# Kernel tuning notes

Measured on AMD Instinct MI355X. Metric: run time of the kernel, lower is better.

## Reference

```python
import jax, jax.numpy as jnp
import numpy as np

N, E, F, H, C, G = 100000, 1000000, 64, 64, 10, 256


def setup_inputs() -> dict:
    key = jax.random.key(0)
    ks = jax.random.split(key, 16)
    s = 1.0 / np.sqrt(F)
    sh = 1.0 / np.sqrt(H)
    return {
        "x": jax.random.normal(ks[0], (N, F), dtype=jnp.float32),
        "edge_index": jax.random.randint(ks[1], (2, E), 0, N, dtype=jnp.int32),
        "edge_attr": jax.random.uniform(ks[2], (E,), dtype=jnp.float32),
        "batch": jnp.sort(jax.random.randint(ks[3], (N,), 0, G, dtype=jnp.int32)),
        "W1r": jax.random.uniform(ks[4], (F, H), minval=-s, maxval=s),
        "W1s": jax.random.uniform(ks[5], (F, H), minval=-s, maxval=s),
        "b1": jax.random.uniform(ks[6], (H,), minval=-s, maxval=s),
        "W2r": jax.random.uniform(ks[7], (H, H), minval=-sh, maxval=sh),
        "W2s": jax.random.uniform(ks[8], (H, H), minval=-sh, maxval=sh),
        "b2": jax.random.uniform(ks[9], (H,), minval=-sh, maxval=sh),
        "W3r": jax.random.uniform(ks[10], (H, H), minval=-sh, maxval=sh),
        "W3s": jax.random.uniform(ks[11], (H, H), minval=-sh, maxval=sh),
        "b3": jax.random.uniform(ks[12], (H,), minval=-sh, maxval=sh),
        "Wl": jax.random.uniform(ks[13], (H, C), minval=-sh, maxval=sh),
        "bl": jax.random.uniform(ks[14], (C,), minval=-sh, maxval=sh),
    }


def graph_conv(x, src, dst, ew, W_rel, W_root, b):
    # gather neighbor feats, weight per-edge, scatter-add to destination
    msgs = x[src] * ew[:, None]                              # [E, F]
    agg = jax.ops.segment_sum(msgs, dst, num_segments=N)     # [N, F]
    return agg @ W_rel + x @ W_root + b                      # [N, H]


def reference(x, edge_index, edge_attr, batch,
              W1r, W1s, b1, W2r, W2s, b2, W3r, W3s, b3, Wl, bl):
    src, dst = edge_index[0], edge_index[1]
    h = jax.nn.relu(graph_conv(x, src, dst, edge_attr, W1r, W1s, b1))
    h = jax.nn.relu(graph_conv(h, src, dst, edge_attr, W2r, W2s, b2))
    h = jax.nn.relu(graph_conv(h, src, dst, edge_attr, W3r, W3s, b3))
    # global mean pool over graphs in the batch
    sums = jax.ops.segment_sum(h, batch, num_segments=G)      # [G, H]
    cnts = jax.ops.segment_sum(jnp.ones((N,), h.dtype), batch, num_segments=G)
    pooled = sums / jnp.maximum(cnts, 1.0)[:, None]
    # dropout is identity in eval mode
    return pooled @ Wl + bl                                   # [G, C]
```

## Files before the change

kernel.cpp:

```cpp
#include <hip/hip_runtime.h>


#define GCN_F 64
#define GCN_C 10
#define CB_SHIFT 9
#define CB_NODES 512
#define NCB_MAX 200
#define CAP 7168
#define SC_CHUNK 2048

typedef __attribute__((ext_vector_type(8))) short bf16x8;
typedef __attribute__((ext_vector_type(4))) float f32x4;

__device__ __forceinline__ unsigned short f2b(float v) {
    union { float f; unsigned int u; } c; c.f = v;
    unsigned int u = c.u;
    return (unsigned short)((u + 0x7FFFu + ((u >> 16) & 1u)) >> 16);
}
__device__ __forceinline__ float b2f(unsigned short u) {
    union { unsigned int u; float f; } c; c.u = ((unsigned int)u) << 16; return c.f;
}

__global__ __launch_bounds__(256) void cvtz_kernel(const float* __restrict__ in,
                                                   unsigned short* __restrict__ out,
                                                   int n4, int* __restrict__ zp, int zn) {
    int gid = blockIdx.x * 256 + threadIdx.x;
    if (gid < zn) zp[gid] = 0;
    int stride = gridDim.x * 256;
    for (int i = gid; i < n4; i += stride) {
        float4 v = reinterpret_cast<const float4*>(in)[i];
        ushort4 o;
        o.x = f2b(v.x); o.y = f2b(v.y); o.z = f2b(v.z); o.w = f2b(v.w);
        reinterpret_cast<ushort4*>(out)[i] = o;
    }
}

__global__ __launch_bounds__(256) void histC_kernel(const int* __restrict__ dst,
                                                    int* __restrict__ bcnt,
                                                    int E, int NCB) {
    __shared__ int h[NCB_MAX];
    int tid = threadIdx.x;
    for (int i = tid; i < NCB; i += 256) h[i] = 0;
    __syncthreads();
    int e0 = blockIdx.x * 4096 + tid;
#pragma unroll
    for (int k = 0; k < 16; ++k) {
        int e = e0 + k * 256;
        if (e < E) atomicAdd(&h[dst[e] >> CB_SHIFT], 1);
    }
    __syncthreads();
    for (int i = tid; i < NCB; i += 256)
        if (h[i]) atomicAdd(&bcnt[i], h[i]);
}

__global__ void bscan_kernel(const int* __restrict__ bcnt, int* __restrict__ gstart,
                             int nb) {
    int lane = threadIdx.x;
    int carry = 0;
    for (int base = 0; base < nb; base += 64) {
        int i = base + lane;
        int v = (i < nb) ? bcnt[i] : 0;
        int sc = v;
#pragma unroll
        for (int off = 1; off < 64; off <<= 1) {
            int t = __shfl_up(sc, off);
            if (lane >= off) sc += t;
        }
        if (i < nb) gstart[i] = carry + sc - v;
        carry += __shfl(sc, 63);
    }
    if (lane == 0) gstart[nb] = carry;
}

__global__ __launch_bounds__(256) void scatterC_kernel(
    const int* __restrict__ src, const int* __restrict__ dst,
    const float* __restrict__ ew, const int* __restrict__ gstart,
    int* __restrict__ gcursor, int2* __restrict__ ebufA, int E, int NCB) {
    __shared__ int2 recS[SC_CHUNK];
    __shared__ int gdest[SC_CHUNK];
    __shared__ int hist[NCB_MAX];
    __shared__ int lstart[NCB_MAX];
    __shared__ int gbase[NCB_MAX];
    __shared__ int cur[NCB_MAX];
    __shared__ int sb[256];

    int tid = threadIdx.x;
    int base = blockIdx.x * SC_CHUNK;
    int m = min(SC_CHUNK, E - base);

    for (int i = tid; i < NCB; i += 256) hist[i] = 0;
    __syncthreads();

    int2 rec[8];
    int bk[8];
#pragma unroll
    for (int k = 0; k < 8; ++k) {
        int e = base + k * 256 + tid;
        if (e < E) {
            int d = dst[e];
            bk[k] = d >> CB_SHIFT;
            rec[k] = make_int2(src[e] | ((d & (CB_NODES - 1)) << 17),
                               __float_as_int(ew[e]));
            atomicAdd(&hist[bk[k]], 1);
        } else bk[k] = -1;
    }
    __syncthreads();

    int v = (tid < NCB) ? hist[tid] : 0;
    sb[tid] = v;
    __syncthreads();
    for (int o = 1; o < 256; o <<= 1) {
        int t = (tid >= o) ? sb[tid - o] : 0;
        __syncthreads();
        sb[tid] += t;
        __syncthreads();
    }
    if (tid < NCB) {
        int excl = sb[tid] - v;
        lstart[tid] = excl;
        cur[tid] = excl;
        gbase[tid] = (v > 0) ? atomicAdd(&gcursor[tid], v) : 0;
    }
    __syncthreads();

#pragma unroll
    for (int k = 0; k < 8; ++k) {
        if (bk[k] >= 0) {
            int p = atomicAdd(&cur[bk[k]], 1);
            recS[p] = rec[k];
            gdest[p] = gstart[bk[k]] + gbase[bk[k]] + (p - lstart[bk[k]]);
        }
    }
    __syncthreads();

    for (int i = tid; i < m; i += 256) ebufA[gdest[i]] = recS[i];
}

__global__ __launch_bounds__(256) void sortCB_kernel(
    const int2* __restrict__ ebufA, const int* __restrict__ gstart,
    int2* __restrict__ ebufS, int* __restrict__ offsets, int N, int E) {
    __shared__ int2 rec[CAP];
    __shared__ int cnt[CB_NODES];
    __shared__ int cur[CB_NODES];
    __shared__ int sbuf[256];
    int cb = blockIdx.x, tid = threadIdx.x;
    int e0 = gstart[cb], e1 = gstart[cb + 1];
    int m = min(e1 - e0, CAP);

    for (int i = tid; i < m; i += 256) rec[i] = ebufA[e0 + i];
    for (int i = tid; i < CB_NODES; i += 256) cnt[i] = 0;
    __syncthreads();
    for (int i = tid; i < m; i += 256)
        atomicAdd(&cnt[(unsigned)rec[i].x >> 17], 1);
    __syncthreads();

    int c0 = cnt[2 * tid], c1 = cnt[2 * tid + 1];
    int part = c0 + c1;
    sbuf[tid] = part;
    __syncthreads();
    for (int off = 1; off < 256; off <<= 1) {
        int t = (tid >= off) ? sbuf[tid - off] : 0;
        __syncthreads();
        sbuf[tid] += t;
        __syncthreads();
    }
    int excl = sbuf[tid] - part;
    int pre0 = excl, pre1 = excl + c0;
    cur[2 * tid] = pre0;
    cur[2 * tid + 1] = pre1;
    int g0 = cb * CB_NODES + 2 * tid;
    if (g0 <= N)     offsets[g0]     = e0 + pre0;
    if (g0 + 1 <= N) offsets[g0 + 1] = e0 + pre1;
    __syncthreads();

    for (int i = tid; i < m; i += 256) {
        int d9 = (unsigned)rec[i].x >> 17;
        int pos = atomicAdd(&cur[d9], 1);
        ebufS[e0 + pos] = make_int2(rec[i].x & 0x1FFFF, rec[i].y);
    }
}

__global__ __launch_bounds__(512) void layer_kernel(
    const unsigned short* __restrict__ xin, const int* __restrict__ offsets,
    const int2* __restrict__ ebufS, const float* __restrict__ Wr,
    const float* __restrict__ Ws, const float* __restrict__ b,
    unsigned short* __restrict__ out, int n)
{
    __shared__ __align__(16) unsigned short bfrag[2][2][4][64][8];
    __shared__ __align__(16) unsigned short aggS[8][16][72];
    int tid = threadIdx.x, lane = tid & 63, wave = tid >> 6;

    for (int i = tid; i < 8192; i += 512) {
        int op = i >> 12;
        int ks = (i >> 11) & 1;
        int ct = (i >> 9) & 3;
        int l  = (i >> 3) & 63;
        int j  = i & 7;
        int k   = ks * 32 + (l >> 4) * 8 + j;
        int col = ct * 16 + (l & 15);
        const float* W = op ? Ws : Wr;
        ((unsigned short*)bfrag)[i] = f2b(W[k * GCN_F + col]);
    }
    __syncthreads();

    int l8 = lane & 7;
    int grp = lane >> 3;
    int gbase = (lane & 56) << 2;
    int wbase = blockIdx.x * 128 + wave * 16;

#pragma unroll
    for (int half = 0; half < 2; ++half) {
        int node = wbase + half * 8 + grp;
        bool nv = node < n;
        int p0 = 0, p1 = 0;
        if (nv) { p0 = offsets[node]; p1 = offsets[node + 1]; }
        float acc[8] = {0.f, 0.f, 0.f, 0.f, 0.f, 0.f, 0.f, 0.f};

        int idx = p0 + l8;
        bool v = idx < p1;
        if (__any(v)) {
            int2 er = ebufS[v ? idx : 0];
            int s  = v ? er.x : 0;
            int wb = v ? er.y : 0;

            for (int c = 1;; ++c) {
                int idxn = p0 + c * 8 + l8;
                bool vn = idxn < p1;
                int2 ern = ebufS[vn ? idxn : 0];

                int sj[8], wj[8];
#pragma unroll
                for (int j = 0; j < 8; ++j) {
                    sj[j] = __builtin_amdgcn_ds_bpermute(gbase + (j << 2), s);
                    wj[j] = __builtin_amdgcn_ds_bpermute(gbase + (j << 2), wb);
                }
                int4 r[8];
#pragma unroll
                for (int j = 0; j < 8; ++j)
                    r[j] = *reinterpret_cast<const int4*>(
                        xin + ((size_t)sj[j] << 6) + l8 * 8);
#pragma unroll
                for (int j = 0; j < 8; ++j) {
                    float wf = __int_as_float(wj[j]);
                    acc[0] = fmaf(__int_as_float(r[j].x << 16),        wf, acc[0]);
                    acc[1] = fmaf(__int_as_float(r[j].x & 0xFFFF0000), wf, acc[1]);
                    acc[2] = fmaf(__int_as_float(r[j].y << 16),        wf, acc[2]);
                    acc[3] = fmaf(__int_as_float(r[j].y & 0xFFFF0000), wf, acc[3]);
                    acc[4] = fmaf(__int_as_float(r[j].z << 16),        wf, acc[4]);
                    acc[5] = fmaf(__int_as_float(r[j].z & 0xFFFF0000), wf, acc[5]);
                    acc[6] = fmaf(__int_as_float(r[j].w << 16),        wf, acc[6]);
                    acc[7] = fmaf(__int_as_float(r[j].w & 0xFFFF0000), wf, acc[7]);
                }

                if (!__any(vn)) break;
                s  = vn ? ern.x : 0;
                wb = vn ? ern.y : 0;
            }
        }

        int4 o;
        o.x = (int)f2b(acc[0]) | ((int)f2b(acc[1]) << 16);
        o.y = (int)f2b(acc[2]) | ((int)f2b(acc[3]) << 16);
        o.z = (int)f2b(acc[4]) | ((int)f2b(acc[5]) << 16);
        o.w = (int)f2b(acc[6]) | ((int)f2b(acc[7]) << 16);
        *reinterpret_cast<int4*>(&aggS[wave][half * 8 + grp][l8 * 8]) = o;
    }

    int l15 = lane & 15, lhi = lane >> 4;

    bf16x8 B[2][2][4];
#pragma unroll
    for (int op = 0; op < 2; ++op)
#pragma unroll
        for (int ks = 0; ks < 2; ++ks)
#pragma unroll
            for (int ct = 0; ct < 4; ++ct)
                B[op][ks][ct] = *reinterpret_cast<const bf16x8*>(&bfrag[op][ks][ct][lane][0]);

    float bias[4];
#pragma unroll
    for (int ct = 0; ct < 4; ++ct) bias[ct] = b[ct * 16 + l15];

    bf16x8 a0 = *reinterpret_cast<const bf16x8*>(&aggS[wave][l15][lhi * 8]);
    bf16x8 a1 = *reinterpret_cast<const bf16x8*>(&aggS[wave][l15][32 + lhi * 8]);
    const unsigned short* xp = xin + (size_t)min(wbase + l15, n - 1) * GCN_F + lhi * 8;
    bf16x8 x0 = *reinterpret_cast<const bf16x8*>(xp);
    bf16x8 x1 = *reinterpret_cast<const bf16x8*>(xp + 32);

#pragma unroll
    for (int ct = 0; ct < 4; ++ct) {
        f32x4 acc = {0.f, 0.f, 0.f, 0.f};
        acc = __builtin_amdgcn_mfma_f32_16x16x32_bf16(a0, B[0][0][ct], acc, 0, 0, 0);
        acc = __builtin_amdgcn_mfma_f32_16x16x32_bf16(a1, B[0][1][ct], acc, 0, 0, 0);
        acc = __builtin_amdgcn_mfma_f32_16x16x32_bf16(x0, B[1][0][ct], acc, 0, 0, 0);
        acc = __builtin_amdgcn_mfma_f32_16x16x32_bf16(x1, B[1][1][ct], acc, 0, 0, 0);
        int col = ct * 16 + l15;
#pragma unroll
        for (int r = 0; r < 4; ++r) {
            int orow = wbase + lhi * 4 + r;
            if (orow < n) {
                float v = fmaxf(acc[r] + bias[ct], 0.f);
                out[(size_t)orow * GCN_F + col] = f2b(v);
            }
        }
    }
}

__global__ __launch_bounds__(256) void pool_kernel(
    const unsigned short* __restrict__ h, const int* __restrict__ batch,
    const float* __restrict__ Wl, const float* __restrict__ bl,
    float* __restrict__ out, int n)
{
    int g    = blockIdx.x;
    int tid  = threadIdx.x;
    int lane = tid & 63;
    int wave = tid >> 6;

    int i0, i1;
    {
        int lo = 0, hi = n;
        while (lo < hi) { int mid = (lo + hi) >> 1; if (batch[mid] < g) lo = mid + 1; else hi = mid; }
        i0 = lo;
        lo = i0; hi = n;
        while (lo < hi) { int mid = (lo + hi) >> 1; if (batch[mid] < g + 1) lo = mid + 1; else hi = mid; }
        i1 = lo;
    }

    float s = 0.f;
    for (int i = i0 + wave; i < i1; i += 4) s += b2f(h[(size_t)i * GCN_F + lane]);

    __shared__ float sp[4][GCN_F];
    sp[wave][lane] = s;
    __syncthreads();
    if (wave == 0) {
        float tot = sp[0][lane] + sp[1][lane] + sp[2][lane] + sp[3][lane];
        float cntf = (float)(i1 - i0);
        sp[0][lane] = tot / fmaxf(cntf, 1.f);
    }
    __syncthreads();
    if (tid < GCN_C) {
        float o = bl[tid];
#pragma unroll
        for (int j = 0; j < GCN_F; ++j) o += sp[0][j] * Wl[j * GCN_C + tid];
        out[g * GCN_C + tid] = o;
    }
}

extern "C" void kernel_launch(void* const* d_in, const int* in_sizes, int n_in,
                              void* d_out, int out_size, void* d_ws, size_t ws_size,
                              hipStream_t stream) {
    const float* x     = (const float*)d_in[0];
    const int*   ei    = (const int*)d_in[1];
    const float* ew    = (const float*)d_in[2];
    const int*   batch = (const int*)d_in[3];
    const float* W1r   = (const float*)d_in[4];
    const float* W1s   = (const float*)d_in[5];
    const float* b1    = (const float*)d_in[6];
    const float* W2r   = (const float*)d_in[7];
    const float* W2s   = (const float*)d_in[8];
    const float* b2    = (const float*)d_in[9];
    const float* W3r   = (const float*)d_in[10];
    const float* W3s   = (const float*)d_in[11];
    const float* b3    = (const float*)d_in[12];
    const float* Wl    = (const float*)d_in[13];
    const float* bl    = (const float*)d_in[14];
    float* out = (float*)d_out;

    const int N = in_sizes[0] / GCN_F;
    const int E = in_sizes[2];
    const int G = out_size / GCN_C;
    const int NCB = (N + CB_NODES - 1) / CB_NODES;

    const int* src = ei;
    const int* dst = ei + E;

    char* ws = (char*)d_ws;
    size_t off = 0;
    size_t csz = ((size_t)NCB * 4 + 15) & ~(size_t)15;
    int* bcnt    = (int*)(ws + off);  off += csz;
    int* gcursor = (int*)(ws + off);  off += csz;
    int* gstart  = (int*)(ws + off);  off += ((size_t)(NCB + 1) * 4 + 15) & ~(size_t)15;
    int* offsets = (int*)(ws + off);  off += ((size_t)(N + 1) * 4 + 15) & ~(size_t)15;
    int2* ebufA  = (int2*)(ws + off); off += (size_t)E * 8;
    int2* ebufS  = (int2*)(ws + off); off += (size_t)E * 8;
    unsigned short* buf0 = (unsigned short*)(ws + off); off += (size_t)N * GCN_F * 2;
    unsigned short* buf1 = (unsigned short*)(ws + off); off += (size_t)N * GCN_F * 2;

    int hblocks = (E + 4095) / 4096;
    int sblocks = (E + SC_CHUNK - 1) / SC_CHUNK;
    int zcount  = (int)(csz * 2 / 4);

    cvtz_kernel<<<1024, 256, 0, stream>>>(x, buf0, N * GCN_F / 4, bcnt, zcount);
    histC_kernel<<<hblocks, 256, 0, stream>>>(dst, bcnt, E, NCB);
    bscan_kernel<<<1, 64, 0, stream>>>(bcnt, gstart, NCB);
    scatterC_kernel<<<sblocks, 256, 0, stream>>>(src, dst, ew, gstart, gcursor, ebufA, E, NCB);
    sortCB_kernel<<<NCB, 256, 0, stream>>>(ebufA, gstart, ebufS, offsets, N, E);

    const int LBLK = (N + 127) / 128;
    layer_kernel<<<LBLK, 512, 0, stream>>>(buf0, offsets, ebufS, W1r, W1s, b1, buf1, N);
    layer_kernel<<<LBLK, 512, 0, stream>>>(buf1, offsets, ebufS, W2r, W2s, b2, buf0, N);
    layer_kernel<<<LBLK, 512, 0, stream>>>(buf0, offsets, ebufS, W3r, W3s, b3, buf1, N);

    pool_kernel<<<G, 256, 0, stream>>>(buf1, batch, Wl, bl, out, N);
}
```

Before: 233.1 us.

## Drop histogram/scan with fixed-capacity buckets and persistent work-stealing layer kernel

Removes the histogram and scan kernels by giving each 512-node destination bucket a fixed CAP-sized slot, so the scatter kernel uses only per-bucket atomic cursors and sortCB records each bucket's end. The layer kernel becomes persistent: 768 blocks whose waves pull 16-node groups from a global atomic counter, which balances uneven degrees and cuts block launch overhead. The intent is fewer launches in preprocessing and better load balance during aggregation. The cost is extra atomics and a padded edge buffer, and a bucket holding more than CAP edges would silently drop edges (the old code also capped at CAP).

```diff
diff --git a/kernel.cpp b/kernel.cpp
--- a/kernel.cpp
+++ b/kernel.cpp
@@ -35,46 +35,9 @@
     }
 }
 
-__global__ __launch_bounds__(256) void histC_kernel(const int* __restrict__ dst,
-                                                    int* __restrict__ bcnt,
-                                                    int E, int NCB) {
-    __shared__ int h[NCB_MAX];
-    int tid = threadIdx.x;
-    for (int i = tid; i < NCB; i += 256) h[i] = 0;
-    __syncthreads();
-    int e0 = blockIdx.x * 4096 + tid;
-#pragma unroll
-    for (int k = 0; k < 16; ++k) {
-        int e = e0 + k * 256;
-        if (e < E) atomicAdd(&h[dst[e] >> CB_SHIFT], 1);
-    }
-    __syncthreads();
-    for (int i = tid; i < NCB; i += 256)
-        if (h[i]) atomicAdd(&bcnt[i], h[i]);
-}
-
-__global__ void bscan_kernel(const int* __restrict__ bcnt, int* __restrict__ gstart,
-                             int nb) {
-    int lane = threadIdx.x;
-    int carry = 0;
-    for (int base = 0; base < nb; base += 64) {
-        int i = base + lane;
-        int v = (i < nb) ? bcnt[i] : 0;
-        int sc = v;
-#pragma unroll
-        for (int off = 1; off < 64; off <<= 1) {
-            int t = __shfl_up(sc, off);
-            if (lane >= off) sc += t;
-        }
-        if (i < nb) gstart[i] = carry + sc - v;
-        carry += __shfl(sc, 63);
-    }
-    if (lane == 0) gstart[nb] = carry;
-}
-
 __global__ __launch_bounds__(256) void scatterC_kernel(
     const int* __restrict__ src, const int* __restrict__ dst,
-    const float* __restrict__ ew, const int* __restrict__ gstart,
+    const float* __restrict__ ew,
     int* __restrict__ gcursor, int2* __restrict__ ebufA, int E, int NCB) {
     __shared__ int2 recS[SC_CHUNK];
     __shared__ int gdest[SC_CHUNK];
@@ -128,7 +91,7 @@
         if (bk[k] >= 0) {
             int p = atomicAdd(&cur[bk[k]], 1);
             recS[p] = rec[k];
-            gdest[p] = gstart[bk[k]] + gbase[bk[k]] + (p - lstart[bk[k]]);
+            gdest[p] = bk[k] * CAP + gbase[bk[k]] + (p - lstart[bk[k]]);
         }
     }
     __syncthreads();
@@ -137,15 +100,17 @@
 }
 
 __global__ __launch_bounds__(256) void sortCB_kernel(
-    const int2* __restrict__ ebufA, const int* __restrict__ gstart,
-    int2* __restrict__ ebufS, int* __restrict__ offsets, int N, int E) {
+    const int2* __restrict__ ebufA, const int* __restrict__ gcursor,
+    int2* __restrict__ ebufS, int* __restrict__ offsets, int* __restrict__ bend,
+    int N, int E) {
     __shared__ int2 rec[CAP];
     __shared__ int cnt[CB_NODES];
     __shared__ int cur[CB_NODES];
     __shared__ int sbuf[256];
     int cb = blockIdx.x, tid = threadIdx.x;
-    int e0 = gstart[cb], e1 = gstart[cb + 1];
-    int m = min(e1 - e0, CAP);
+    int e0 = cb * CAP;
+    int m = min(gcursor[cb], CAP);
+    if (tid == 0) bend[cb] = e0 + m;
 
     for (int i = tid; i < m; i += 256) rec[i] = ebufA[e0 + i];
     for (int i = tid; i < CB_NODES; i += 256) cnt[i] = 0;
@@ -182,9 +147,10 @@
 
 __global__ __launch_bounds__(512) void layer_kernel(
     const unsigned short* __restrict__ xin, const int* __restrict__ offsets,
-    const int2* __restrict__ ebufS, const float* __restrict__ Wr,
-    const float* __restrict__ Ws, const float* __restrict__ b,
-    unsigned short* __restrict__ out, int n)
+    const int* __restrict__ bend, const int2* __restrict__ ebufS,
+    const float* __restrict__ Wr, const float* __restrict__ Ws,
+    const float* __restrict__ b, unsigned short* __restrict__ out,
+    int* __restrict__ stealc, int ngroups, int n)
 {
     __shared__ __align__(16) unsigned short bfrag[2][2][4][64][8];
     __shared__ __align__(16) unsigned short aggS[8][16][72];
@@ -206,66 +172,6 @@
     int l8 = lane & 7;
     int grp = lane >> 3;
     int gbase = (lane & 56) << 2;
-    int wbase = blockIdx.x * 128 + wave * 16;
-
-#pragma unroll
-    for (int half = 0; half < 2; ++half) {
-        int node = wbase + half * 8 + grp;
-        bool nv = node < n;
-        int p0 = 0, p1 = 0;
-        if (nv) { p0 = offsets[node]; p1 = offsets[node + 1]; }
-        float acc[8] = {0.f, 0.f, 0.f, 0.f, 0.f, 0.f, 0.f, 0.f};
-
-        int idx = p0 + l8;
-        bool v = idx < p1;
-        if (__any(v)) {
-            int2 er = ebufS[v ? idx : 0];
-            int s  = v ? er.x : 0;
-            int wb = v ? er.y : 0;
-
-            for (int c = 1;; ++c) {
-                int idxn = p0 + c * 8 + l8;
-                bool vn = idxn < p1;
-                int2 ern = ebufS[vn ? idxn : 0];
-
-                int sj[8], wj[8];
-#pragma unroll
-                for (int j = 0; j < 8; ++j) {
-                    sj[j] = __builtin_amdgcn_ds_bpermute(gbase + (j << 2), s);
-                    wj[j] = __builtin_amdgcn_ds_bpermute(gbase + (j << 2), wb);
-                }
-                int4 r[8];
-#pragma unroll
-                for (int j = 0; j < 8; ++j)
-                    r[j] = *reinterpret_cast<const int4*>(
-                        xin + ((size_t)sj[j] << 6) + l8 * 8);
-#pragma unroll
-                for (int j = 0; j < 8; ++j) {
-                    float wf = __int_as_float(wj[j]);
-                    acc[0] = fmaf(__int_as_float(r[j].x << 16),        wf, acc[0]);
-                    acc[1] = fmaf(__int_as_float(r[j].x & 0xFFFF0000), wf, acc[1]);
-                    acc[2] = fmaf(__int_as_float(r[j].y << 16),        wf, acc[2]);
-                    acc[3] = fmaf(__int_as_float(r[j].y & 0xFFFF0000), wf, acc[3]);
-                    acc[4] = fmaf(__int_as_float(r[j].z << 16),        wf, acc[4]);
-                    acc[5] = fmaf(__int_as_float(r[j].z & 0xFFFF0000), wf, acc[5]);
-                    acc[6] = fmaf(__int_as_float(r[j].w << 16),        wf, acc[6]);
-                    acc[7] = fmaf(__int_as_float(r[j].w & 0xFFFF0000), wf, acc[7]);
-                }
-
-                if (!__any(vn)) break;
-                s  = vn ? ern.x : 0;
-                wb = vn ? ern.y : 0;
-            }
-        }
-
-        int4 o;
-        o.x = (int)f2b(acc[0]) | ((int)f2b(acc[1]) << 16);
-        o.y = (int)f2b(acc[2]) | ((int)f2b(acc[3]) << 16);
-        o.z = (int)f2b(acc[4]) | ((int)f2b(acc[5]) << 16);
-        o.w = (int)f2b(acc[6]) | ((int)f2b(acc[7]) << 16);
-        *reinterpret_cast<int4*>(&aggS[wave][half * 8 + grp][l8 * 8]) = o;
-    }
-
     int l15 = lane & 15, lhi = lane >> 4;
 
     bf16x8 B[2][2][4];
@@ -281,26 +187,96 @@
 #pragma unroll
     for (int ct = 0; ct < 4; ++ct) bias[ct] = b[ct * 16 + l15];
 
-    bf16x8 a0 = *reinterpret_cast<const bf16x8*>(&aggS[wave][l15][lhi * 8]);
-    bf16x8 a1 = *reinterpret_cast<const bf16x8*>(&aggS[wave][l15][32 + lhi * 8]);
-    const unsigned short* xp = xin + (size_t)min(wbase + l15, n - 1) * GCN_F + lhi * 8;
-    bf16x8 x0 = *reinterpret_cast<const bf16x8*>(xp);
-    bf16x8 x1 = *reinterpret_cast<const bf16x8*>(xp + 32);
-
-#pragma unroll
-    for (int ct = 0; ct < 4; ++ct) {
-        f32x4 acc = {0.f, 0.f, 0.f, 0.f};
-        acc = __builtin_amdgcn_mfma_f32_16x16x32_bf16(a0, B[0][0][ct], acc, 0, 0, 0);
-        acc = __builtin_amdgcn_mfma_f32_16x16x32_bf16(a1, B[0][1][ct], acc, 0, 0, 0);
-        acc = __builtin_amdgcn_mfma_f32_16x16x32_bf16(x0, B[1][0][ct], acc, 0, 0, 0);
-        acc = __builtin_amdgcn_mfma_f32_16x16x32_bf16(x1, B[1][1][ct], acc, 0, 0, 0);
-        int col = ct * 16 + l15;
-#pragma unroll
-        for (int r = 0; r < 4; ++r) {
-            int orow = wbase + lhi * 4 + r;
-            if (orow < n) {
-                float v = fmaxf(acc[r] + bias[ct], 0.f);
-                out[(size_t)orow * GCN_F + col] = f2b(v);
+    for (;;) {
+        int gsel = 0;
+        if (lane == 0) gsel = atomicAdd(stealc, 1);
+        gsel = __builtin_amdgcn_readfirstlane(gsel);
+        if (gsel >= ngroups) break;
+        int wbase = gsel * 16;
+
+#pragma unroll
+        for (int half = 0; half < 2; ++half) {
+            int node = wbase + half * 8 + grp;
+            bool nv = node < n;
+            int p0 = 0, p1 = 0;
+            if (nv) {
+                p0 = offsets[node];
+                p1 = ((node & (CB_NODES - 1)) == CB_NODES - 1)
+                         ? bend[node >> CB_SHIFT] : offsets[node + 1];
+            }
+            float acc[8] = {0.f, 0.f, 0.f, 0.f, 0.f, 0.f, 0.f, 0.f};
+
+            int idx = p0 + l8;
+            bool v = idx < p1;
+            if (__any(v)) {
+                int2 er = ebufS[v ? idx : 0];
+                int s  = v ? er.x : 0;
+                int wb = v ? er.y : 0;
+
+                for (int c = 1;; ++c) {
+                    int idxn = p0 + c * 8 + l8;
+                    bool vn = idxn < p1;
+                    int2 ern = ebufS[vn ? idxn : 0];
+
+                    int sj[8], wj[8];
+#pragma unroll
+                    for (int j = 0; j < 8; ++j) {
+                        sj[j] = __builtin_amdgcn_ds_bpermute(gbase + (j << 2), s);
+                        wj[j] = __builtin_amdgcn_ds_bpermute(gbase + (j << 2), wb);
+                    }
+                    int4 r[8];
+#pragma unroll
+                    for (int j = 0; j < 8; ++j)
+                        r[j] = *reinterpret_cast<const int4*>(
+                            xin + ((size_t)sj[j] << 6) + l8 * 8);
+#pragma unroll
+                    for (int j = 0; j < 8; ++j) {
+                        float wf = __int_as_float(wj[j]);
+                        acc[0] = fmaf(__int_as_float(r[j].x << 16),        wf, acc[0]);
+                        acc[1] = fmaf(__int_as_float(r[j].x & 0xFFFF0000), wf, acc[1]);
+                        acc[2] = fmaf(__int_as_float(r[j].y << 16),        wf, acc[2]);
+                        acc[3] = fmaf(__int_as_float(r[j].y & 0xFFFF0000), wf, acc[3]);
+                        acc[4] = fmaf(__int_as_float(r[j].z << 16),        wf, acc[4]);
+                        acc[5] = fmaf(__int_as_float(r[j].z & 0xFFFF0000), wf, acc[5]);
+                        acc[6] = fmaf(__int_as_float(r[j].w << 16),        wf, acc[6]);
+                        acc[7] = fmaf(__int_as_float(r[j].w & 0xFFFF0000), wf, acc[7]);
+                    }
+
+                    if (!__any(vn)) break;
+                    s  = vn ? ern.x : 0;
+                    wb = vn ? ern.y : 0;
+                }
+            }
+
+            int4 o;
+            o.x = (int)f2b(acc[0]) | ((int)f2b(acc[1]) << 16);
+            o.y = (int)f2b(acc[2]) | ((int)f2b(acc[3]) << 16);
+            o.z = (int)f2b(acc[4]) | ((int)f2b(acc[5]) << 16);
+            o.w = (int)f2b(acc[6]) | ((int)f2b(acc[7]) << 16);
+            *reinterpret_cast<int4*>(&aggS[wave][half * 8 + grp][l8 * 8]) = o;
+        }
+
+        bf16x8 a0 = *reinterpret_cast<const bf16x8*>(&aggS[wave][l15][lhi * 8]);
+        bf16x8 a1 = *reinterpret_cast<const bf16x8*>(&aggS[wave][l15][32 + lhi * 8]);
+        const unsigned short* xp = xin + (size_t)min(wbase + l15, n - 1) * GCN_F + lhi * 8;
+        bf16x8 x0 = *reinterpret_cast<const bf16x8*>(xp);
+        bf16x8 x1 = *reinterpret_cast<const bf16x8*>(xp + 32);
+
+#pragma unroll
+        for (int ct = 0; ct < 4; ++ct) {
+            f32x4 acc = {0.f, 0.f, 0.f, 0.f};
+            acc = __builtin_amdgcn_mfma_f32_16x16x32_bf16(a0, B[0][0][ct], acc, 0, 0, 0);
+            acc = __builtin_amdgcn_mfma_f32_16x16x32_bf16(a1, B[0][1][ct], acc, 0, 0, 0);
+            acc = __builtin_amdgcn_mfma_f32_16x16x32_bf16(x0, B[1][0][ct], acc, 0, 0, 0);
+            acc = __builtin_amdgcn_mfma_f32_16x16x32_bf16(x1, B[1][1][ct], acc, 0, 0, 0);
+            int col = ct * 16 + l15;
+#pragma unroll
+            for (int r = 0; r < 4; ++r) {
+                int orow = wbase + lhi * 4 + r;
+                if (orow < n) {
+                    float v = fmaxf(acc[r] + bias[ct], 0.f);
+                    out[(size_t)orow * GCN_F + col] = f2b(v);
+                }
             }
         }
     }
@@ -370,6 +346,7 @@
     const int E = in_sizes[2];
     const int G = out_size / GCN_C;
     const int NCB = (N + CB_NODES - 1) / CB_NODES;
+    const int NGROUPS = (N + 15) / 16;
 
     const int* src = ei;
     const int* dst = ei + E;
@@ -377,29 +354,29 @@
     char* ws = (char*)d_ws;
     size_t off = 0;
     size_t csz = ((size_t)NCB * 4 + 15) & ~(size_t)15;
-    int* bcnt    = (int*)(ws + off);  off += csz;
     int* gcursor = (int*)(ws + off);  off += csz;
-    int* gstart  = (int*)(ws + off);  off += ((size_t)(NCB + 1) * 4 + 15) & ~(size_t)15;
+    int* stealc  = (int*)(ws + off);  off += 16;
+    int* bend    = (int*)(ws + off);  off += csz;
     int* offsets = (int*)(ws + off);  off += ((size_t)(N + 1) * 4 + 15) & ~(size_t)15;
-    int2* ebufA  = (int2*)(ws + off); off += (size_t)E * 8;
-    int2* ebufS  = (int2*)(ws + off); off += (size_t)E * 8;
+    int2* ebufA  = (int2*)(ws + off); off += (size_t)NCB * CAP * 8;
+    int2* ebufS  = (int2*)(ws + off); off += (size_t)NCB * CAP * 8;
     unsigned short* buf0 = (unsigned short*)(ws + off); off += (size_t)N * GCN_F * 2;
     unsigned short* buf1 = (unsigned short*)(ws + off); off += (size_t)N * GCN_F * 2;
 
-    int hblocks = (E + 4095) / 4096;
     int sblocks = (E + SC_CHUNK - 1) / SC_CHUNK;
-    int zcount  = (int)(csz * 2 / 4);
-
-    cvtz_kernel<<<1024, 256, 0, stream>>>(x, buf0, N * GCN_F / 4, bcnt, zcount);
-    histC_kernel<<<hblocks, 256, 0, stream>>>(dst, bcnt, E, NCB);
-    bscan_kernel<<<1, 64, 0, stream>>>(bcnt, gstart, NCB);
-    scatterC_kernel<<<sblocks, 256, 0, stream>>>(src, dst, ew, gstart, gcursor, ebufA, E, NCB);
-    sortCB_kernel<<<NCB, 256, 0, stream>>>(ebufA, gstart, ebufS, offsets, N, E);
-
-    const int LBLK = (N + 127) / 128;
-    layer_kernel<<<LBLK, 512, 0, stream>>>(buf0, offsets, ebufS, W1r, W1s, b1, buf1, N);
-    layer_kernel<<<LBLK, 512, 0, stream>>>(buf1, offsets, ebufS, W2r, W2s, b2, buf0, N);
-    layer_kernel<<<LBLK, 512, 0, stream>>>(buf0, offsets, ebufS, W3r, W3s, b3, buf1, N);
+    int zcount  = (int)(csz / 4) + 4;
+
+    cvtz_kernel<<<1024, 256, 0, stream>>>(x, buf0, N * GCN_F / 4, gcursor, zcount);
+    scatterC_kernel<<<sblocks, 256, 0, stream>>>(src, dst, ew, gcursor, ebufA, E, NCB);
+    sortCB_kernel<<<NCB, 256, 0, stream>>>(ebufA, gcursor, ebufS, offsets, bend, N, E);
+
+    const int LBLK = 768;
+    layer_kernel<<<LBLK, 512, 0, stream>>>(buf0, offsets, bend, ebufS, W1r, W1s, b1,
+                                           buf1, stealc + 0, NGROUPS, N);
+    layer_kernel<<<LBLK, 512, 0, stream>>>(buf1, offsets, bend, ebufS, W2r, W2s, b2,
+                                           buf0, stealc + 1, NGROUPS, N);
+    layer_kernel<<<LBLK, 512, 0, stream>>>(buf0, offsets, bend, ebufS, W3r, W3s, b3,
+                                           buf1, stealc + 2, NGROUPS, N);
 
     pool_kernel<<<G, 256, 0, stream>>>(buf1, batch, Wl, bl, out, N);
 }
```

Result: slower. 543.3 us (+133.1%).
